# Kernel tuning notes

Measured on AMD Instinct MI355X. Metric: run time of the kernel, lower is better.

## Reference

```python
import jax, jax.numpy as jnp
import numpy as np


def setup_inputs() -> dict:
    key = jax.random.key(0)
    k1, k2 = jax.random.split(key)
    embeddings = jax.random.normal(k1, (32, 512, 1024), dtype=jnp.float32)
    aspect = jax.random.normal(k2, (32, 1024), dtype=jnp.float32)
    return {"embeddings": embeddings, "aspect": aspect}


def reference(embeddings, aspect):
    # go_backwards=False, so no sequence reversal.
    # L2-normalize embeddings per token and aspect per sample.
    e = embeddings / jnp.linalg.norm(embeddings, axis=2, keepdims=True)
    a = aspect / jnp.linalg.norm(aspect, axis=1, keepdims=True)
    # NaN-mask (zero-norm rows produce NaN after division).
    e = jnp.where(jnp.isnan(e), jnp.zeros_like(e), e)
    a = jnp.where(jnp.isnan(a), jnp.zeros_like(a), a)
    # Circulant matrix: circ[b, i, j] = a[b, (j - i) mod D]
    # (matches the TF scatter_nd construction M[i, (i+k)%D] = a[k]).
    D = e.shape[-1]
    r = jnp.arange(D)
    idx = (r[None, :] - r[:, None]) % D  # [D, D]
    circ = a[:, idx]  # [B, D, D]
    # matmul(e, circ, transpose_b=True): out[b,s,i] = sum_j e[b,s,j] * circ[b,i,j]
    return jnp.einsum('bsd,bid->bsi', e, circ)
```

## Files before the change

kernel.cpp:

```cpp
#include <hip/hip_runtime.h>
#include <hip/hip_bf16.h>

typedef __attribute__((ext_vector_type(8))) short bf16x8;
typedef __attribute__((ext_vector_type(4))) float f32x4;

#define NB 32
#define NS 512
#define ND 1024

__device__ __forceinline__ unsigned short f2bf(float f) {
  unsigned int u = __float_as_uint(f);
  u = (u + 0x7FFFu + ((u >> 16) & 1u)) >> 16;
  return (unsigned short)u;
}

__global__ __launch_bounds__(256)
void enormbf_fused_kernel(const float* __restrict__ emb,
                          unsigned short* __restrict__ eN,
                          const float* __restrict__ aspect,
                          unsigned short* __restrict__ a_n) {
  int wave = threadIdx.x >> 6, lane = threadIdx.x & 63;
  size_t row = (size_t)blockIdx.x * 4 + wave;
  const float4* p = (const float4*)(emb + row * ND);
  float4 v[4];
  float s = 0.f;
#pragma unroll
  for (int j = 0; j < 4; ++j) {
    v[j] = p[lane + 64 * j];
    s += v[j].x * v[j].x + v[j].y * v[j].y + v[j].z * v[j].z + v[j].w * v[j].w;
  }
#pragma unroll
  for (int off = 32; off >= 1; off >>= 1) s += __shfl_xor(s, off);
  float inv = (s > 0.f) ? (1.f / sqrtf(s)) : 0.f;
  ushort4* o = (ushort4*)(eN + row * ND);
#pragma unroll
  for (int j = 0; j < 4; ++j) {
    ushort4 u;
    u.x = f2bf(v[j].x * inv); u.y = f2bf(v[j].y * inv);
    u.z = f2bf(v[j].z * inv); u.w = f2bf(v[j].w * inv);
    o[lane + 64 * j] = u;
  }

  if (blockIdx.x < NB) {
    int b = blockIdx.x;
    int t = threadIdx.x;
    const float4* pa = (const float4*)(aspect + (size_t)b * ND);
    float4 va = pa[t];
    float sa = va.x * va.x + va.y * va.y + va.z * va.z + va.w * va.w;
#pragma unroll
    for (int off = 32; off >= 1; off >>= 1) sa += __shfl_down(sa, off);
    __shared__ float red[4];
    if ((t & 63) == 0) red[t >> 6] = sa;
    __syncthreads();
    float tot = red[0] + red[1] + red[2] + red[3];
    float inva = (tot > 0.f) ? (1.f / sqrtf(tot)) : 0.f;
    ushort4 u;
    u.x = f2bf(va.x * inva); u.y = f2bf(va.y * inva);
    u.z = f2bf(va.z * inva); u.w = f2bf(va.w * inva);
    ((ushort4*)(a_n + (size_t)b * ND))[t] = u;
  }
}

__global__ __launch_bounds__(512, 2)
void corr_gemm5_kernel(const unsigned short* __restrict__ eN,
                       const unsigned short* __restrict__ a_n,
                       float* __restrict__ out) {
  __shared__ __align__(16) unsigned short Alds[3 * 16384];
  __shared__ __align__(16) unsigned short copies[8 * 1288];

  const int b = blockIdx.x, mt = blockIdx.y, nt = blockIdx.z;
  const int n0 = nt * 256, m0 = mt * 256;
  const int tid = threadIdx.x;

  const int lane = tid & 63, wv = tid >> 6;
  const int wm = wv >> 2, wn = wv & 3;
  const int q = lane >> 4, l16 = lane & 15;
  const int mx = l16 & 7;
  const int s00 = (q ^ mx) * 8;
  const int s01 = ((4 + q) ^ mx) * 8;
  const int arow = (wm * 128 + l16) * 64;

  const int pB = (8 - mx) & 7;
  const unsigned short* Bp = copies + pB * 1287 + (256 + 8 * q - wn * 64 - l16);

  const unsigned short* gstage =
      eN + ((size_t)b * NS + m0 + (tid >> 3)) * ND + (size_t)(((tid & 7) ^ ((tid >> 3) & 7)) * 8);
  char* ldsAbase = (char*)Alds;

  unsigned short av[20];
  {
    const unsigned short* an = a_n + (size_t)b * ND;
    const int p = tid & 7;
    const int x0 = (tid >> 3) * 20;
    const int base = (768 - n0 + p) & 1023;
#pragma unroll
    for (int j = 0; j < 20; ++j) av[j] = an[(base + x0 + j) & 1023];
  }

#pragma unroll
  for (int j = 0; j < 4; ++j)
    __builtin_amdgcn_global_load_lds(
        (const __attribute__((address_space(1))) void*)(gstage + (size_t)j * 64 * ND),
        (__attribute__((address_space(3))) void*)(ldsAbase + (size_t)tid * 16 + j * 8192),
        16, 0, 0);
#pragma unroll
  for (int j = 0; j < 4; ++j)
    __builtin_amdgcn_global_load_lds(
        (const __attribute__((address_space(1))) void*)(gstage + (size_t)j * 64 * ND + 64),
        (__attribute__((address_space(3))) void*)(ldsAbase + 32768 + (size_t)tid * 16 + j * 8192),
        16, 0, 0);

  {
    const int p = tid & 7;
    const int x0 = (tid >> 3) * 20;
#pragma unroll
    for (int j = 0; j < 20; ++j) copies[p * 1288 + x0 + j] = av[j];
  }

  f32x4 acc[8][4];
#pragma unroll
  for (int i = 0; i < 8; ++i)
#pragma unroll
    for (int j = 0; j < 4; ++j)
      acc[i][j] = (f32x4){0.f, 0.f, 0.f, 0.f};

  asm volatile("s_waitcnt lgkmcnt(0)" ::: "memory");
  __builtin_amdgcn_s_barrier();
  asm volatile("s_waitcnt vmcnt(4)" ::: "memory");
  __builtin_amdgcn_s_barrier();

  bf16x8 a0[4], a1[4], bfr[4][2];

#define ISSUE_A(DST, BASE, PHN)                                          \
  do {                                                                   \
    DST[0] = *(const bf16x8*)&(BASE)[arow + (PHN) * 2048 + s00];         \
    DST[1] = *(const bf16x8*)&(BASE)[arow + (PHN) * 2048 + s01];         \
    DST[2] = *(const bf16x8*)&(BASE)[arow + (PHN) * 2048 + 1024 + s00];  \
    DST[3] = *(const bf16x8*)&(BASE)[arow + (PHN) * 2048 + 1024 + s01];  \
  } while (0)

#define STAGE_PAIR(J0)                                                                   \
  do {                                                                                   \
    if (kt + 2 < 16) {                                                                   \
      const unsigned short* sg_ = gstage + (size_t)(kt + 2) * 64;                        \
      char* dl_ = ldsAbase + c2 * 32768 + (size_t)tid * 16;                              \
      __builtin_amdgcn_global_load_lds(                                                  \
          (const __attribute__((address_space(1))) void*)(sg_ + (size_t)(J0) * 64 * ND), \
          (__attribute__((address_space(3))) void*)(dl_ + (J0) * 8192), 16, 0, 0);       \
      __builtin_amdgcn_global_load_lds(                                                  \
          (const __attribute__((address_space(1))) void*)(sg_ + (size_t)((J0) + 1) * 64 * ND), \
          (__attribute__((address_space(3))) void*)(dl_ + ((J0) + 1) * 8192), 16, 0, 0); \
    }                                                                                    \
  } while (0)

#define MFMA_PH(PH, CS)                                                                       \
  do {                                                                                        \
    __builtin_amdgcn_s_setprio(1);                                                            \
    _Pragma("unroll")                                                                         \
    for (int n = 0; n < 4; ++n) {                                                             \
      acc[2*(PH)][n]   = __builtin_amdgcn_mfma_f32_16x16x32_bf16(CS[0], bfr[n][0], acc[2*(PH)][n],   0, 0, 0); \
      acc[2*(PH)][n]   = __builtin_amdgcn_mfma_f32_16x16x32_bf16(CS[1], bfr[n][1], acc[2*(PH)][n],   0, 0, 0); \
      acc[2*(PH)+1][n] = __builtin_amdgcn_mfma_f32_16x16x32_bf16(CS[2], bfr[n][0], acc[2*(PH)+1][n], 0, 0, 0); \
      acc[2*(PH)+1][n] = __builtin_amdgcn_mfma_f32_16x16x32_bf16(CS[3], bfr[n][1], acc[2*(PH)+1][n], 0, 0, 0); \
    }                                                                                         \
    __builtin_amdgcn_s_setprio(0);                                                            \
  } while (0)

  int c0 = 0, c1 = 1, c2 = 2;

  ISSUE_A(a0, Alds, 0);

#pragma unroll 1
  for (int kt = 0; kt < 16; ++kt) {
    const unsigned short* At = Alds + c0 * 16384;
    const unsigned short* An = Alds + c1 * 16384;

    {
      const unsigned short* Bt = Bp + kt * 64;
#pragma unroll
      for (int n = 0; n < 4; ++n) {
        bfr[n][0] = *(const bf16x8*)(Bt - n * 16);
        bfr[n][1] = *(const bf16x8*)(Bt + 32 - n * 16);
      }
    }
    __builtin_amdgcn_sched_barrier(0);
    ISSUE_A(a1, At, 1);
    STAGE_PAIR(0);
    __builtin_amdgcn_sched_barrier(0);
    __builtin_amdgcn_s_barrier();
    asm volatile("s_waitcnt lgkmcnt(4)" ::: "memory");
    __builtin_amdgcn_sched_barrier(0);
    MFMA_PH(0, a0);

    ISSUE_A(a0, At, 2);
    STAGE_PAIR(2);
    if (kt < 14) {
      asm volatile("s_waitcnt vmcnt(4)" ::: "memory");
    } else {
      asm volatile("s_waitcnt vmcnt(0)" ::: "memory");
    }
    __builtin_amdgcn_sched_barrier(0);
    __builtin_amdgcn_s_barrier();
    asm volatile("s_waitcnt lgkmcnt(4)" ::: "memory");
    __builtin_amdgcn_sched_barrier(0);
    MFMA_PH(1, a1);

    ISSUE_A(a1, At, 3);
    __builtin_amdgcn_sched_barrier(0);
    __builtin_amdgcn_s_barrier();
    asm volatile("s_waitcnt lgkmcnt(4)" ::: "memory");
    __builtin_amdgcn_sched_barrier(0);
    MFMA_PH(2, a0);

    if (kt < 15) {
      ISSUE_A(a0, An, 0);
      __builtin_amdgcn_sched_barrier(0);
      __builtin_amdgcn_s_barrier();
      asm volatile("s_waitcnt lgkmcnt(4)" ::: "memory");
    } else {
      __builtin_amdgcn_s_barrier();
      asm volatile("s_waitcnt lgkmcnt(0)" ::: "memory");
    }
    __builtin_amdgcn_sched_barrier(0);
    MFMA_PH(3, a1);
    __builtin_amdgcn_s_barrier();

    int tmp = c0; c0 = c1; c1 = c2; c2 = tmp;
  }
#undef MFMA_PH
#undef STAGE_PAIR
#undef ISSUE_A

  float* outB = out + ((size_t)b * NS + m0) * ND + n0;
#pragma unroll
  for (int i = 0; i < 8; ++i) {
#pragma unroll
    for (int rg = 0; rg < 4; ++rg) {
      int r = wm * 128 + i * 16 + q * 4 + rg;
      float* orow = outB + (size_t)r * ND + wn * 64 + l16;
#pragma unroll
      for (int n = 0; n < 4; ++n)
        orow[n * 16] = acc[i][n][rg];
    }
  }
}

__global__ void anorm_kernel(const float* __restrict__ aspect,
                             unsigned short* __restrict__ a_n) {
  int b = blockIdx.x;
  int t = threadIdx.x;
  const float4* p = (const float4*)(aspect + (size_t)b * ND);
  float4 v = p[t];
  float s = v.x * v.x + v.y * v.y + v.z * v.z + v.w * v.w;
#pragma unroll
  for (int off = 32; off >= 1; off >>= 1) s += __shfl_down(s, off);
  __shared__ float red[4];
  if ((t & 63) == 0) red[t >> 6] = s;
  __syncthreads();
  float tot = red[0] + red[1] + red[2] + red[3];
  float inv = (tot > 0.f) ? (1.f / sqrtf(tot)) : 0.f;
  ushort4 u;
  u.x = f2bf(v.x * inv); u.y = f2bf(v.y * inv);
  u.z = f2bf(v.z * inv); u.w = f2bf(v.w * inv);
  ((ushort4*)(a_n + (size_t)b * ND))[t] = u;
}

__global__ void enorm_kernel(const float* __restrict__ emb,
                             float* __restrict__ inv_norm) {
  int wave = threadIdx.x >> 6;
  int lane = threadIdx.x & 63;
  int row = blockIdx.x * 4 + wave;
  const float4* p = (const float4*)(emb + (size_t)row * ND);
  float s = 0.f;
#pragma unroll
  for (int j = 0; j < 4; ++j) {
    float4 v = p[lane + 64 * j];
    s += v.x * v.x + v.y * v.y + v.z * v.z + v.w * v.w;
  }
#pragma unroll
  for (int off = 32; off >= 1; off >>= 1) s += __shfl_down(s, off);
  if (lane == 0) inv_norm[row] = (s > 0.f) ? (1.f / sqrtf(s)) : 0.f;
}

__global__ __launch_bounds__(256)
void corr_gemm_kernel(const float* __restrict__ emb,
                      const float* __restrict__ inv_norm,
                      const unsigned short* __restrict__ a_n,
                      float* __restrict__ out) {
  __shared__ unsigned short copies[8][2056];
  __shared__ unsigned short Atile[128][40];

  const int nt = blockIdx.x, mt = blockIdx.y, b = blockIdx.z;
  const int n0 = nt * 128, m0 = mt * 128;
  const int t = threadIdx.x;

  {
    const unsigned short* an = a_n + (size_t)b * ND;
    int p = t & 7;
    int x0 = (t >> 3) * 64;
#pragma unroll
    for (int j = 0; j < 64; j += 4) {
      ushort4 u;
      u.x = an[(x0 + j + 0 + p) & 1023];
      u.y = an[(x0 + j + 1 + p) & 1023];
      u.z = an[(x0 + j + 2 + p) & 1023];
      u.w = an[(x0 + j + 3 + p) & 1023];
      *(ushort4*)&copies[p][x0 + j] = u;
    }
  }

  const int ar = t >> 3;
  const int ac = (t & 7) * 4;
  float invn[4];
#pragma unroll
  for (int w = 0; w < 4; ++w)
    invn[w] = inv_norm[b * NS + m0 + ar + 32 * w];

  const int lane = t & 63;
  const int wv = t >> 6;
  const int wm = wv >> 1, wn = wv & 1;
  const int q = lane >> 4, l16 = lane & 15;

  f32x4 acc[4][4];
#pragma unroll
  for (int i = 0; i < 4; ++i)
#pragma unroll
    for (int j = 0; j < 4; ++j)
      acc[i][j] = (f32x4){0.f, 0.f, 0.f, 0.f};

  const float* embB = emb + ((size_t)b * NS + m0) * ND;

  for (int k0 = 0; k0 < ND; k0 += 32) {
    __syncthreads();
#pragma unroll
    for (int w = 0; w < 4; ++w) {
      int r = ar + 32 * w;
      float4 v = *(const float4*)(embB + (size_t)r * ND + k0 + ac);
      float in = invn[w];
      ushort4 u;
      u.x = f2bf(v.x * in); u.y = f2bf(v.y * in);
      u.z = f2bf(v.z * in); u.w = f2bf(v.w * in);
      *(ushort4*)&Atile[r][ac] = u;
    }
    __syncthreads();

    bf16x8 af[4], bfr[4];
#pragma unroll
    for (int r = 0; r < 4; ++r) {
      int m = wm * 64 + r * 16 + l16;
      af[r] = *(const bf16x8*)&Atile[m][q * 8];
    }
#pragma unroll
    for (int r = 0; r < 4; ++r) {
      int ng = n0 + wn * 64 + r * 16 + l16;
      int e0 = k0 + 8 * q - ng + 1024;
      int p = e0 & 7;
      bfr[r] = *(const bf16x8*)&copies[p][e0 - p];
    }
#pragma unroll
    for (int i = 0; i < 4; ++i)
#pragma unroll
      for (int j = 0; j < 4; ++j)
        acc[i][j] = __builtin_amdgcn_mfma_f32_16x16x32_bf16(af[i], bfr[j], acc[i][j], 0, 0, 0);
  }

  float* outB = out + ((size_t)b * NS + m0) * ND + n0;
#pragma unroll
  for (int i = 0; i < 4; ++i) {
#pragma unroll
    for (int rg = 0; rg < 4; ++rg) {
      int s = wm * 64 + i * 16 + q * 4 + rg;
      float* orow = outB + (size_t)s * ND + wn * 64 + l16;
#pragma unroll
      for (int j = 0; j < 4; ++j)
        orow[j * 16] = acc[i][j][rg];
    }
  }
}

extern "C" void kernel_launch(void* const* d_in, const int* in_sizes, int n_in,
                              void* d_out, int out_size, void* d_ws, size_t ws_size,
                              hipStream_t stream) {
  const float* emb = (const float*)d_in[0];
  const float* aspect = (const float*)d_in[1];
  float* out = (float*)d_out;

  const size_t need = 65536 + (size_t)NB * NS * ND * 2;

  if (ws_size >= need) {
    unsigned short* a_n = (unsigned short*)d_ws;
    unsigned short* eN = (unsigned short*)((char*)d_ws + 65536);
    enormbf_fused_kernel<<<4096, 256, 0, stream>>>(emb, eN, aspect, a_n);
    corr_gemm5_kernel<<<dim3(NB, 2, 4), 512, 0, stream>>>(eN, a_n, out);
  } else {
    float* inv_norm = (float*)d_ws;
    unsigned short* a_n = (unsigned short*)((char*)d_ws + 65536);
    enorm_kernel<<<4096, 256, 0, stream>>>(emb, inv_norm);
    anorm_kernel<<<NB, 256, 0, stream>>>(aspect, a_n);
    corr_gemm_kernel<<<dim3(8, 4, NB), 256, 0, stream>>>(emb, inv_norm, a_n, out);
  }
}
```

Measured before the change: 141.0 us.

## Load GEMM A operand directly from global memory, drop LDS staging

The circulant GEMM kernel no longer stages the normalized embedding tile through a triple-buffered LDS ring with async global-to-LDS loads and barriers. Each wave now reads its A fragments straight from global memory into registers, and the block tile shrinks to 128x256 with 256 threads, so the grid doubles to 512 blocks. This removes the barriers and LDS traffic for A and raises block count. In exchange, the four waves in a block each fetch the same A rows separately, relying on cache, and global-load latency is hidden only by software prefetch of one phase ahead.

```diff
diff --git a/kernel.cpp b/kernel.cpp
--- a/kernel.cpp
+++ b/kernel.cpp
@@ -61,61 +61,41 @@
   }
 }
 
-__global__ __launch_bounds__(512, 2)
-void corr_gemm5_kernel(const unsigned short* __restrict__ eN,
+__global__ __launch_bounds__(256, 2)
+void corr_gemm6_kernel(const unsigned short* __restrict__ eN,
                        const unsigned short* __restrict__ a_n,
                        float* __restrict__ out) {
-  __shared__ __align__(16) unsigned short Alds[3 * 16384];
   __shared__ __align__(16) unsigned short copies[8 * 1288];
 
   const int b = blockIdx.x, mt = blockIdx.y, nt = blockIdx.z;
-  const int n0 = nt * 256, m0 = mt * 256;
+  const int n0 = nt * 256, m0 = mt * 128;
   const int tid = threadIdx.x;
 
-  const int lane = tid & 63, wv = tid >> 6;
-  const int wm = wv >> 2, wn = wv & 3;
+  const int lane = tid & 63, wn = tid >> 6;
   const int q = lane >> 4, l16 = lane & 15;
   const int mx = l16 & 7;
-  const int s00 = (q ^ mx) * 8;
-  const int s01 = ((4 + q) ^ mx) * 8;
-  const int arow = (wm * 128 + l16) * 64;
-
-  const int pB = (8 - mx) & 7;
-  const unsigned short* Bp = copies + pB * 1287 + (256 + 8 * q - wn * 64 - l16);
-
-  const unsigned short* gstage =
-      eN + ((size_t)b * NS + m0 + (tid >> 3)) * ND + (size_t)(((tid & 7) ^ ((tid >> 3) & 7)) * 8);
-  char* ldsAbase = (char*)Alds;
-
-  unsigned short av[20];
+
   {
     const unsigned short* an = a_n + (size_t)b * ND;
     const int p = tid & 7;
-    const int x0 = (tid >> 3) * 20;
+    const int x0 = (tid >> 3) * 40;
     const int base = (768 - n0 + p) & 1023;
 #pragma unroll
-    for (int j = 0; j < 20; ++j) av[j] = an[(base + x0 + j) & 1023];
-  }
-
-#pragma unroll
-  for (int j = 0; j < 4; ++j)
-    __builtin_amdgcn_global_load_lds(
-        (const __attribute__((address_space(1))) void*)(gstage + (size_t)j * 64 * ND),
-        (__attribute__((address_space(3))) void*)(ldsAbase + (size_t)tid * 16 + j * 8192),
-        16, 0, 0);
-#pragma unroll
-  for (int j = 0; j < 4; ++j)
-    __builtin_amdgcn_global_load_lds(
-        (const __attribute__((address_space(1))) void*)(gstage + (size_t)j * 64 * ND + 64),
-        (__attribute__((address_space(3))) void*)(ldsAbase + 32768 + (size_t)tid * 16 + j * 8192),
-        16, 0, 0);
-
-  {
-    const int p = tid & 7;
-    const int x0 = (tid >> 3) * 20;
-#pragma unroll
-    for (int j = 0; j < 20; ++j) copies[p * 1288 + x0 + j] = av[j];
-  }
+    for (int j = 0; j < 40; j += 4) {
+      ushort4 u;
+      u.x = an[(base + x0 + j + 0) & 1023];
+      u.y = an[(base + x0 + j + 1) & 1023];
+      u.z = an[(base + x0 + j + 2) & 1023];
+      u.w = an[(base + x0 + j + 3) & 1023];
+      *(ushort4*)&copies[p * 1288 + x0 + j] = u;
+    }
+  }
+  __syncthreads();
+
+  const int pB = (8 - mx) & 7;
+  const unsigned short* Bp = copies + pB * 1287 + (256 + 8 * q - wn * 64 - l16);
+
+  const unsigned short* Abase = eN + ((size_t)b * NS + m0 + l16) * ND + q * 8;
 
   f32x4 acc[8][4];
 #pragma unroll
@@ -124,33 +104,25 @@
     for (int j = 0; j < 4; ++j)
       acc[i][j] = (f32x4){0.f, 0.f, 0.f, 0.f};
 
-  asm volatile("s_waitcnt lgkmcnt(0)" ::: "memory");
-  __builtin_amdgcn_s_barrier();
-  asm volatile("s_waitcnt vmcnt(4)" ::: "memory");
-  __builtin_amdgcn_s_barrier();
-
   bf16x8 a0[4], a1[4], bfr[4][2];
 
-#define ISSUE_A(DST, BASE, PHN)                                          \
-  do {                                                                   \
-    DST[0] = *(const bf16x8*)&(BASE)[arow + (PHN) * 2048 + s00];         \
-    DST[1] = *(const bf16x8*)&(BASE)[arow + (PHN) * 2048 + s01];         \
-    DST[2] = *(const bf16x8*)&(BASE)[arow + (PHN) * 2048 + 1024 + s00];  \
-    DST[3] = *(const bf16x8*)&(BASE)[arow + (PHN) * 2048 + 1024 + s01];  \
+#define ISSUE_A(DST, RB, KTT)                                       \
+  do {                                                              \
+    const unsigned short* _p = Abase + (size_t)(RB) * (16 * ND) + (KTT) * 64; \
+    DST[0] = *(const bf16x8*)(_p);                                  \
+    DST[1] = *(const bf16x8*)(_p + 32);                             \
+    DST[2] = *(const bf16x8*)(_p + 16 * ND);                        \
+    DST[3] = *(const bf16x8*)(_p + 16 * ND + 32);                   \
   } while (0)
 
-#define STAGE_PAIR(J0)                                                                   \
-  do {                                                                                   \
-    if (kt + 2 < 16) {                                                                   \
-      const unsigned short* sg_ = gstage + (size_t)(kt + 2) * 64;                        \
-      char* dl_ = ldsAbase + c2 * 32768 + (size_t)tid * 16;                              \
-      __builtin_amdgcn_global_load_lds(                                                  \
-          (const __attribute__((address_space(1))) void*)(sg_ + (size_t)(J0) * 64 * ND), \
-          (__attribute__((address_space(3))) void*)(dl_ + (J0) * 8192), 16, 0, 0);       \
-      __builtin_amdgcn_global_load_lds(                                                  \
-          (const __attribute__((address_space(1))) void*)(sg_ + (size_t)((J0) + 1) * 64 * ND), \
-          (__attribute__((address_space(3))) void*)(dl_ + ((J0) + 1) * 8192), 16, 0, 0); \
-    }                                                                                    \
+#define LOAD_B(KTT)                                                 \
+  do {                                                              \
+    const unsigned short* Bt = Bp + (KTT) * 64;                     \
+    _Pragma("unroll")                                               \
+    for (int n = 0; n < 4; ++n) {                                   \
+      bfr[n][0] = *(const bf16x8*)(Bt - n * 16);                    \
+      bfr[n][1] = *(const bf16x8*)(Bt + 32 - n * 16);               \
+    }                                                               \
   } while (0)
 
 #define MFMA_PH(PH, CS)                                                                       \
@@ -166,69 +138,25 @@
     __builtin_amdgcn_s_setprio(0);                                                            \
   } while (0)
 
-  int c0 = 0, c1 = 1, c2 = 2;
-
-  ISSUE_A(a0, Alds, 0);
+  ISSUE_A(a0, 0, 0);
+  LOAD_B(0);
 
 #pragma unroll 1
   for (int kt = 0; kt < 16; ++kt) {
-    const unsigned short* At = Alds + c0 * 16384;
-    const unsigned short* An = Alds + c1 * 16384;
-
-    {
-      const unsigned short* Bt = Bp + kt * 64;
-#pragma unroll
-      for (int n = 0; n < 4; ++n) {
-        bfr[n][0] = *(const bf16x8*)(Bt - n * 16);
-        bfr[n][1] = *(const bf16x8*)(Bt + 32 - n * 16);
-      }
-    }
+    ISSUE_A(a1, 2, kt);
+    MFMA_PH(0, a0);
+    ISSUE_A(a0, 4, kt);
+    MFMA_PH(1, a1);
+    ISSUE_A(a1, 6, kt);
+    MFMA_PH(2, a0);
+    const int ktn = (kt < 15) ? kt + 1 : 15;
+    ISSUE_A(a0, 0, ktn);
+    MFMA_PH(3, a1);
     __builtin_amdgcn_sched_barrier(0);
-    ISSUE_A(a1, At, 1);
-    STAGE_PAIR(0);
-    __builtin_amdgcn_sched_barrier(0);
-    __builtin_amdgcn_s_barrier();
-    asm volatile("s_waitcnt lgkmcnt(4)" ::: "memory");
-    __builtin_amdgcn_sched_barrier(0);
-    MFMA_PH(0, a0);
-
-    ISSUE_A(a0, At, 2);
-    STAGE_PAIR(2);
-    if (kt < 14) {
-      asm volatile("s_waitcnt vmcnt(4)" ::: "memory");
-    } else {
-      asm volatile("s_waitcnt vmcnt(0)" ::: "memory");
-    }
-    __builtin_amdgcn_sched_barrier(0);
-    __builtin_amdgcn_s_barrier();
-    asm volatile("s_waitcnt lgkmcnt(4)" ::: "memory");
-    __builtin_amdgcn_sched_barrier(0);
-    MFMA_PH(1, a1);
-
-    ISSUE_A(a1, At, 3);
-    __builtin_amdgcn_sched_barrier(0);
-    __builtin_amdgcn_s_barrier();
-    asm volatile("s_waitcnt lgkmcnt(4)" ::: "memory");
-    __builtin_amdgcn_sched_barrier(0);
-    MFMA_PH(2, a0);
-
-    if (kt < 15) {
-      ISSUE_A(a0, An, 0);
-      __builtin_amdgcn_sched_barrier(0);
-      __builtin_amdgcn_s_barrier();
-      asm volatile("s_waitcnt lgkmcnt(4)" ::: "memory");
-    } else {
-      __builtin_amdgcn_s_barrier();
-      asm volatile("s_waitcnt lgkmcnt(0)" ::: "memory");
-    }
-    __builtin_amdgcn_sched_barrier(0);
-    MFMA_PH(3, a1);
-    __builtin_amdgcn_s_barrier();
-
-    int tmp = c0; c0 = c1; c1 = c2; c2 = tmp;
+    LOAD_B(ktn);
   }
 #undef MFMA_PH
-#undef STAGE_PAIR
+#undef LOAD_B
 #undef ISSUE_A
 
   float* outB = out + ((size_t)b * NS + m0) * ND + n0;
@@ -236,7 +164,7 @@
   for (int i = 0; i < 8; ++i) {
 #pragma unroll
     for (int rg = 0; rg < 4; ++rg) {
-      int r = wm * 128 + i * 16 + q * 4 + rg;
+      int r = i * 16 + q * 4 + rg;
       float* orow = outB + (size_t)r * ND + wn * 64 + l16;
 #pragma unroll
       for (int n = 0; n < 4; ++n)
@@ -391,7 +319,7 @@
     unsigned short* a_n = (unsigned short*)d_ws;
     unsigned short* eN = (unsigned short*)((char*)d_ws + 65536);
     enormbf_fused_kernel<<<4096, 256, 0, stream>>>(emb, eN, aspect, a_n);
-    corr_gemm5_kernel<<<dim3(NB, 2, 4), 512, 0, stream>>>(eN, a_n, out);
+    corr_gemm6_kernel<<<dim3(NB, 4, 4), 256, 0, stream>>>(eN, a_n, out);
   } else {
     float* inv_norm = (float*)d_ws;
     unsigned short* a_n = (unsigned short*)((char*)d_ws + 65536);
```

After: 174.1 us. +23.5%, slower.

## Shrink GEMM tile to 128x256 with 4 waves and one barrier per k-step

Applied to the files above, without the earlier changes.

Halves the M tile of the circulant-correlation GEMM from 256 to 128 rows, using 256-thread blocks of 4 waves instead of 8, and doubles the grid to 512 blocks. The k-loop is restructured to issue all four staging loads for k+2 up front, run the four MFMA phases with only lgkmcnt waits, and synchronise once per k-step instead of at every phase. The aim is better CU occupancy across the 256 CUs and less barrier overhead. The cost is lower reuse of the B (circulant) fragments per block, twice as much redundant circulant-copy setup, and less overlap of LDS reads across phases.

```diff
diff --git a/kernel.cpp b/kernel.cpp
--- a/kernel.cpp
+++ b/kernel.cpp
@@ -61,24 +61,23 @@
   }
 }
 
-__global__ __launch_bounds__(512, 2)
-void corr_gemm5_kernel(const unsigned short* __restrict__ eN,
+__global__ __launch_bounds__(256, 2)
+void corr_gemm8_kernel(const unsigned short* __restrict__ eN,
                        const unsigned short* __restrict__ a_n,
                        float* __restrict__ out) {
-  __shared__ __align__(16) unsigned short Alds[3 * 16384];
+  __shared__ __align__(16) unsigned short Alds[3 * 8192];
   __shared__ __align__(16) unsigned short copies[8 * 1288];
 
   const int b = blockIdx.x, mt = blockIdx.y, nt = blockIdx.z;
-  const int n0 = nt * 256, m0 = mt * 256;
+  const int n0 = nt * 256, m0 = mt * 128;
   const int tid = threadIdx.x;
 
-  const int lane = tid & 63, wv = tid >> 6;
-  const int wm = wv >> 2, wn = wv & 3;
+  const int lane = tid & 63, wn = tid >> 6;
   const int q = lane >> 4, l16 = lane & 15;
   const int mx = l16 & 7;
   const int s00 = (q ^ mx) * 8;
   const int s01 = ((4 + q) ^ mx) * 8;
-  const int arow = (wm * 128 + l16) * 64;
+  const int arow = l16 * 64;
 
   const int pB = (8 - mx) & 7;
   const unsigned short* Bp = copies + pB * 1287 + (256 + 8 * q - wn * 64 - l16);
@@ -87,34 +86,34 @@
       eN + ((size_t)b * NS + m0 + (tid >> 3)) * ND + (size_t)(((tid & 7) ^ ((tid >> 3) & 7)) * 8);
   char* ldsAbase = (char*)Alds;
 
-  unsigned short av[20];
+  unsigned short av[40];
   {
     const unsigned short* an = a_n + (size_t)b * ND;
     const int p = tid & 7;
-    const int x0 = (tid >> 3) * 20;
+    const int x0 = (tid >> 3) * 40;
     const int base = (768 - n0 + p) & 1023;
 #pragma unroll
-    for (int j = 0; j < 20; ++j) av[j] = an[(base + x0 + j) & 1023];
+    for (int j = 0; j < 40; ++j) av[j] = an[(base + x0 + j) & 1023];
   }
 
 #pragma unroll
   for (int j = 0; j < 4; ++j)
     __builtin_amdgcn_global_load_lds(
-        (const __attribute__((address_space(1))) void*)(gstage + (size_t)j * 64 * ND),
-        (__attribute__((address_space(3))) void*)(ldsAbase + (size_t)tid * 16 + j * 8192),
+        (const __attribute__((address_space(1))) void*)(gstage + (size_t)j * 32 * ND),
+        (__attribute__((address_space(3))) void*)(ldsAbase + (size_t)tid * 16 + j * 4096),
         16, 0, 0);
 #pragma unroll
   for (int j = 0; j < 4; ++j)
     __builtin_amdgcn_global_load_lds(
-        (const __attribute__((address_space(1))) void*)(gstage + (size_t)j * 64 * ND + 64),
-        (__attribute__((address_space(3))) void*)(ldsAbase + 32768 + (size_t)tid * 16 + j * 8192),
+        (const __attribute__((address_space(1))) void*)(gstage + (size_t)j * 32 * ND + 64),
+        (__attribute__((address_space(3))) void*)(ldsAbase + 16384 + (size_t)tid * 16 + j * 4096),
         16, 0, 0);
 
   {
     const int p = tid & 7;
-    const int x0 = (tid >> 3) * 20;
-#pragma unroll
-    for (int j = 0; j < 20; ++j) copies[p * 1288 + x0 + j] = av[j];
+    const int x0 = (tid >> 3) * 40;
+#pragma unroll
+    for (int j = 0; j < 40; ++j) copies[p * 1288 + x0 + j] = av[j];
   }
 
   f32x4 acc[8][4];
@@ -125,8 +124,10 @@
       acc[i][j] = (f32x4){0.f, 0.f, 0.f, 0.f};
 
   asm volatile("s_waitcnt lgkmcnt(0)" ::: "memory");
+  __builtin_amdgcn_sched_barrier(0);
   __builtin_amdgcn_s_barrier();
   asm volatile("s_waitcnt vmcnt(4)" ::: "memory");
+  __builtin_amdgcn_sched_barrier(0);
   __builtin_amdgcn_s_barrier();
 
   bf16x8 a0[4], a1[4], bfr[4][2];
@@ -139,18 +140,25 @@
     DST[3] = *(const bf16x8*)&(BASE)[arow + (PHN) * 2048 + 1024 + s01];  \
   } while (0)
 
-#define STAGE_PAIR(J0)                                                                   \
-  do {                                                                                   \
-    if (kt + 2 < 16) {                                                                   \
-      const unsigned short* sg_ = gstage + (size_t)(kt + 2) * 64;                        \
-      char* dl_ = ldsAbase + c2 * 32768 + (size_t)tid * 16;                              \
-      __builtin_amdgcn_global_load_lds(                                                  \
-          (const __attribute__((address_space(1))) void*)(sg_ + (size_t)(J0) * 64 * ND), \
-          (__attribute__((address_space(3))) void*)(dl_ + (J0) * 8192), 16, 0, 0);       \
-      __builtin_amdgcn_global_load_lds(                                                  \
-          (const __attribute__((address_space(1))) void*)(sg_ + (size_t)((J0) + 1) * 64 * ND), \
-          (__attribute__((address_space(3))) void*)(dl_ + ((J0) + 1) * 8192), 16, 0, 0); \
-    }                                                                                    \
+#define STAGE4(SLOT, KTT)                                                              \
+  do {                                                                                 \
+    const unsigned short* sg_ = gstage + (size_t)(KTT) * 64;                           \
+    char* dl_ = ldsAbase + (SLOT) * 16384 + (size_t)tid * 16;                          \
+    _Pragma("unroll")                                                                  \
+    for (int j = 0; j < 4; ++j)                                                        \
+      __builtin_amdgcn_global_load_lds(                                                \
+          (const __attribute__((address_space(1))) void*)(sg_ + (size_t)j * 32 * ND),  \
+          (__attribute__((address_space(3))) void*)(dl_ + j * 4096), 16, 0, 0);        \
+  } while (0)
+
+#define LOAD_B(KTT)                                                 \
+  do {                                                              \
+    const unsigned short* Bt = Bp + (KTT) * 64;                     \
+    _Pragma("unroll")                                               \
+    for (int n = 0; n < 4; ++n) {                                   \
+      bfr[n][0] = *(const bf16x8*)(Bt - n * 16);                    \
+      bfr[n][1] = *(const bf16x8*)(Bt + 32 - n * 16);               \
+    }                                                               \
   } while (0)
 
 #define MFMA_PH(PH, CS)                                                                       \
@@ -168,67 +176,46 @@
 
   int c0 = 0, c1 = 1, c2 = 2;
 
-  ISSUE_A(a0, Alds, 0);
-
 #pragma unroll 1
   for (int kt = 0; kt < 16; ++kt) {
-    const unsigned short* At = Alds + c0 * 16384;
-    const unsigned short* An = Alds + c1 * 16384;
-
-    {
-      const unsigned short* Bt = Bp + kt * 64;
-#pragma unroll
-      for (int n = 0; n < 4; ++n) {
-        bfr[n][0] = *(const bf16x8*)(Bt - n * 16);
-        bfr[n][1] = *(const bf16x8*)(Bt + 32 - n * 16);
-      }
-    }
-    __builtin_amdgcn_sched_barrier(0);
+    const unsigned short* At = Alds + c0 * 8192;
+
+    if (kt + 2 < 16) STAGE4(c2, kt + 2);
+
+    ISSUE_A(a0, At, 0);
+    LOAD_B(kt);
     ISSUE_A(a1, At, 1);
-    STAGE_PAIR(0);
-    __builtin_amdgcn_sched_barrier(0);
-    __builtin_amdgcn_s_barrier();
     asm volatile("s_waitcnt lgkmcnt(4)" ::: "memory");
     __builtin_amdgcn_sched_barrier(0);
     MFMA_PH(0, a0);
 
     ISSUE_A(a0, At, 2);
-    STAGE_PAIR(2);
+    asm volatile("s_waitcnt lgkmcnt(4)" ::: "memory");
+    __builtin_amdgcn_sched_barrier(0);
+    MFMA_PH(1, a1);
+
+    ISSUE_A(a1, At, 3);
+    asm volatile("s_waitcnt lgkmcnt(4)" ::: "memory");
+    __builtin_amdgcn_sched_barrier(0);
+    MFMA_PH(2, a0);
+
+    asm volatile("s_waitcnt lgkmcnt(0)" ::: "memory");
+    __builtin_amdgcn_sched_barrier(0);
+    MFMA_PH(3, a1);
+
     if (kt < 14) {
       asm volatile("s_waitcnt vmcnt(4)" ::: "memory");
-    } else {
+    } else if (kt == 14) {
       asm volatile("s_waitcnt vmcnt(0)" ::: "memory");
     }
     __builtin_amdgcn_sched_barrier(0);
     __builtin_amdgcn_s_barrier();
-    asm volatile("s_waitcnt lgkmcnt(4)" ::: "memory");
-    __builtin_amdgcn_sched_barrier(0);
-    MFMA_PH(1, a1);
-
-    ISSUE_A(a1, At, 3);
-    __builtin_amdgcn_sched_barrier(0);
-    __builtin_amdgcn_s_barrier();
-    asm volatile("s_waitcnt lgkmcnt(4)" ::: "memory");
-    __builtin_amdgcn_sched_barrier(0);
-    MFMA_PH(2, a0);
-
-    if (kt < 15) {
-      ISSUE_A(a0, An, 0);
-      __builtin_amdgcn_sched_barrier(0);
-      __builtin_amdgcn_s_barrier();
-      asm volatile("s_waitcnt lgkmcnt(4)" ::: "memory");
-    } else {
-      __builtin_amdgcn_s_barrier();
-      asm volatile("s_waitcnt lgkmcnt(0)" ::: "memory");
-    }
-    __builtin_amdgcn_sched_barrier(0);
-    MFMA_PH(3, a1);
-    __builtin_amdgcn_s_barrier();
 
     int tmp = c0; c0 = c1; c1 = c2; c2 = tmp;
   }
 #undef MFMA_PH
-#undef STAGE_PAIR
+#undef LOAD_B
+#undef STAGE4
 #undef ISSUE_A
 
   float* outB = out + ((size_t)b * NS + m0) * ND + n0;
@@ -236,7 +223,7 @@
   for (int i = 0; i < 8; ++i) {
 #pragma unroll
     for (int rg = 0; rg < 4; ++rg) {
-      int r = wm * 128 + i * 16 + q * 4 + rg;
+      int r = i * 16 + q * 4 + rg;
       float* orow = outB + (size_t)r * ND + wn * 64 + l16;
 #pragma unroll
       for (int n = 0; n < 4; ++n)
@@ -391,7 +378,7 @@
     unsigned short* a_n = (unsigned short*)d_ws;
     unsigned short* eN = (unsigned short*)((char*)d_ws + 65536);
     enormbf_fused_kernel<<<4096, 256, 0, stream>>>(emb, eN, aspect, a_n);
-    corr_gemm5_kernel<<<dim3(NB, 2, 4), 512, 0, stream>>>(eN, a_n, out);
+    corr_gemm8_kernel<<<dim3(NB, 4, 4), 256, 0, stream>>>(eN, a_n, out);
   } else {
     float* inv_norm = (float*)d_ws;
     unsigned short* a_n = (unsigned short*)((char*)d_ws + 65536);
```

Result: faster. 136.9 us (-2.9%).
